# Kernel tuning notes

Measured on AMD Instinct MI355X. Metric: run time of the kernel, lower is better.

## Reference

```python
import jax, jax.numpy as jnp
import numpy as np

IN_F, OUT_F = 4096, 4096
GROUP = 128
N_GROUPS = IN_F // GROUP
R, NUM_A, NUM_B = 16, 2, 2
LORA_ALPHA = 32
SCALING = LORA_ALPHA / R  # 2.0
BITS = 4
PACK = 32 // BITS  # 8 int4 per int32


def dequant_gptq(qweight, qzeros, scales, g_idx):
    """Unpack int4 GPTQ weights -> dense [in_features, out_features] fp32."""
    shifts = (jnp.arange(PACK, dtype=jnp.int32) * BITS)
    # qweight: [in/8, out] packed along in dim
    wq = (qweight[:, None, :] >> shifts[None, :, None]) & 0xF       # [in/8, 8, out]
    wq = wq.reshape(IN_F, OUT_F).astype(jnp.float32)
    # qzeros: [n_groups, out/8] packed along out dim
    zq = (qzeros[:, :, None] >> shifts[None, None, :]) & 0xF        # [g, out/8, 8]
    zq = zq.reshape(N_GROUPS, OUT_F).astype(jnp.float32)
    # per-row group lookup
    return scales[g_idx] * (wq - zq[g_idx])                          # [in, out]


def activation_weights(x, normalize=True):
    # 'inps' mode: per-input-feature importance from mean |activation|
    w = jnp.mean(jnp.abs(x), axis=tuple(range(x.ndim - 1)))          # [in]
    if normalize:
        w = w / (jnp.mean(w) + 1e-6)
    return w


def setup_inputs() -> dict:
    key = jax.random.key(0)
    ks = jax.random.split(key, 8)
    x = jax.random.normal(ks[0], (2, 2048, IN_F), dtype=jnp.float32)
    scales = jax.random.uniform(ks[1], (N_GROUPS, OUT_F), dtype=jnp.float32) * 0.01 + 0.001
    bias = jax.random.normal(ks[2], (OUT_F,), dtype=jnp.float32) * 0.01
    lora_A = jax.random.normal(ks[3], (NUM_A, R, IN_F), dtype=jnp.float32) * (1.0 / np.sqrt(IN_F))
    lora_B = jax.random.normal(ks[4], (NUM_B, OUT_F, R), dtype=jnp.float32) * 0.01
    qweight = jax.random.randint(ks[5], (IN_F // PACK, OUT_F), 0, 2147483647, dtype=jnp.int32)
    qzeros = jax.random.randint(ks[6], (N_GROUPS, OUT_F // PACK), 0, 2147483647, dtype=jnp.int32)
    g_idx = (jnp.arange(IN_F, dtype=jnp.int32) // GROUP).astype(jnp.int32)
    return {"x": x, "scales": scales, "bias": bias, "lora_A": lora_A,
            "lora_B": lora_B, "qweight": qweight, "qzeros": qzeros, "g_idx": g_idx}


def reference(x, scales, bias, lora_A, lora_B, qweight, qzeros, g_idx):
    W = dequant_gptq(qweight, qzeros, scales, g_idx)                 # [in, out]
    result = jnp.einsum('bsi,io->bso', x, W) + bias                  # base GPTQ linear
    # activation-aware 'inps' weighting (dropout p=0 -> identity, eval mode)
    aw = activation_weights(x, normalize=True)                       # [in]
    x_w = x * aw                                                     # broadcast on last dim
    # sum_{i,j} B_j(A_i(x_w)) == (sum_j B_j) @ (sum_i A_i) @ x_w (all linear, no bias)
    A_sum = jnp.sum(lora_A, axis=0)                                  # [r, in]
    B_sum = jnp.sum(lora_B, axis=0)                                  # [out, r]
    h = jnp.einsum('bsi,ri->bsr', x_w, A_sum)                        # [b, s, r]
    result = result + jnp.einsum('bsr,or->bso', h, B_sum) * SCALING
    return result
```

## Files before the change

kernel.cpp:

```cpp
#include <hip/hip_runtime.h>
#include <stdint.h>

#define IN_F 4096
#define OUT_F 4096

typedef __attribute__((ext_vector_type(4))) float f32x4;
typedef _Float16 f16x8 __attribute__((ext_vector_type(8)));
typedef _Float16 f16x2 __attribute__((ext_vector_type(2)));
typedef unsigned short u16x8 __attribute__((ext_vector_type(8)));

__device__ __forceinline__ unsigned short f2h(float f) {
  _Float16 h = (_Float16)f;
  return __builtin_bit_cast(unsigned short, h);
}

#define SIGMA_TAB 0x73625140u

#define OFF_XH     ((size_t)0)
#define OFF_PART   ((size_t)33554432)
#define OFF_W      ((size_t)35651584)
#define OFF_BSUM   ((size_t)35667968)
#define OFF_AW     ((size_t)35668480)
#define OFF_BS     ((size_t)35799552)
#define OFF_HPART  ((size_t)36061696)
#define OFF_HB     ((size_t)38158848)
#define WS_NEED    ((size_t)38420992)

__global__ __launch_bounds__(256) void k1_prep(const float* __restrict__ x,
                                               unsigned short* __restrict__ xh,
                                               float* __restrict__ part) {
  int t = threadIdx.x;
  int c8 = (blockIdx.x * 256 + t) * 8;
  int by = blockIdx.y;
  float a[8];
  #pragma unroll
  for (int i = 0; i < 8; ++i) a[i] = 0.f;
  for (int rr = 0; rr < 32; ++rr) {
    size_t off = (size_t)(by * 32 + rr) * IN_F + c8;
    f32x4 v0 = *(const f32x4*)(x + off);
    f32x4 v1 = *(const f32x4*)(x + off + 4);
    u16x8 o;
    o[0] = f2h(v0[0]); o[1] = f2h(v1[0]); o[2] = f2h(v0[1]); o[3] = f2h(v1[1]);
    o[4] = f2h(v0[2]); o[5] = f2h(v1[2]); o[6] = f2h(v0[3]); o[7] = f2h(v1[3]);
    *(u16x8*)(xh + off) = o;
    a[0] += fabsf(v0[0]); a[1] += fabsf(v0[1]); a[2] += fabsf(v0[2]); a[3] += fabsf(v0[3]);
    a[4] += fabsf(v1[0]); a[5] += fabsf(v1[1]); a[6] += fabsf(v1[2]); a[7] += fabsf(v1[3]);
  }
  f32x4 p0 = { a[0], a[1], a[2], a[3] };
  f32x4 p1 = { a[4], a[5], a[6], a[7] };
  *(f32x4*)(part + (size_t)by * IN_F + c8) = p0;
  *(f32x4*)(part + (size_t)by * IN_F + c8 + 4) = p1;
}

__global__ __launch_bounds__(256) void k2_colred(const float* __restrict__ part,
                                                 float* __restrict__ w,
                                                 float* __restrict__ bsum) {
  int t = threadIdx.x;
  int col = blockIdx.x * 256 + t;
  float s = 0.f;
  for (int st = 0; st < 128; ++st) s += part[(size_t)st * IN_F + col];
  float wv = s * (1.0f / 4096.0f);
  w[col] = wv;
  __shared__ float red[256];
  red[t] = wv; __syncthreads();
  for (int k = 128; k > 0; k >>= 1) { if (t < k) red[t] += red[t + k]; __syncthreads(); }
  if (t == 0) bsum[blockIdx.x] = red[0];
}

__global__ __launch_bounds__(256) void k3_fold(const float* __restrict__ lora_A,
                                               const float* __restrict__ lora_B,
                                               const float* __restrict__ w,
                                               const float* __restrict__ bsum,
                                               unsigned short* __restrict__ A_w,
                                               unsigned short* __restrict__ Bs) {
  int b = blockIdx.x, t = threadIdx.x;
  float s = 0.f;
  #pragma unroll
  for (int i = 0; i < 16; ++i) s += bsum[i];
  float iv = 1.0f / (s * (1.0f / 4096.0f) + 1e-6f);
  if (b < 256) {
    int idx = b * 256 + t;
    int r = idx >> 12;
    int pos = idx & 4095;
    int p = pos & 7;
    int orig = (pos & ~7) + (int)((SIGMA_TAB >> (p * 4)) & 7);
    float v = (lora_A[(size_t)r * IN_F + orig] + lora_A[(size_t)(16 + r) * IN_F + orig]) * w[orig] * iv;
    A_w[idx] = f2h(v);
  } else {
    int idx = (b - 256) * 256 + t;
    int o = idx >> 5, r = idx & 31;
    float v = 0.f;
    if (r < 16) v = 2.0f * (lora_B[o * 16 + r] + lora_B[OUT_F * 16 + o * 16 + r]);
    Bs[idx] = f2h(v);
  }
}

__global__ __launch_bounds__(256) void k4_h(const unsigned short* __restrict__ xh,
                                            const unsigned short* __restrict__ A_w,
                                            float* __restrict__ hpart) {
  int mb = blockIdx.x, kc = blockIdx.y;
  int t = threadIdx.x, wid = t >> 6, l = t & 63;
  int m0 = mb * 128 + wid * 32;
  int lr = l & 15, lg = l >> 4;
  f32x4 z = { 0.f, 0.f, 0.f, 0.f };
  f32x4 acc0 = z, acc1 = z;
  for (int it = 0; it < 16; ++it) {
    int k = kc * 512 + it * 32 + lg * 8;
    f16x8 b  = *(const f16x8*)(A_w + (size_t)lr * IN_F + k);
    f16x8 a0 = *(const f16x8*)(xh + (size_t)(m0 + lr) * IN_F + k);
    f16x8 a1 = *(const f16x8*)(xh + (size_t)(m0 + 16 + lr) * IN_F + k);
    acc0 = __builtin_amdgcn_mfma_f32_16x16x32_f16(a0, b, acc0, 0, 0, 0);
    acc1 = __builtin_amdgcn_mfma_f32_16x16x32_f16(a1, b, acc1, 0, 0, 0);
  }
  float* hp = hpart + (size_t)kc * IN_F * 16;
  #pragma unroll
  for (int r = 0; r < 4; ++r) {
    hp[(size_t)(m0 + lg * 4 + r) * 16 + lr]      = acc0[r];
    hp[(size_t)(m0 + 16 + lg * 4 + r) * 16 + lr] = acc1[r];
  }
}

__global__ __launch_bounds__(256) void k5_hred(const float* __restrict__ hpart,
                                               unsigned short* __restrict__ hb) {
  int gid = blockIdx.x * 256 + threadIdx.x;
  int m = gid >> 5, r = gid & 31;
  float v = 0.f;
  if (r < 16)
    for (int kc = 0; kc < 8; ++kc) v += hpart[(size_t)kc * 65536 + m * 16 + r];
  hb[gid] = f2h(v);
}

__device__ __forceinline__ f16x8 deq8(unsigned int q, f16x2 s2, f16x2 zz2) {
  unsigned int u0 = ( q         & 0x000F000Fu) | 0x64006400u;
  unsigned int u1 = ((q >> 4)   & 0x000F000Fu) | 0x64006400u;
  unsigned int u2 = ((q >> 8)   & 0x000F000Fu) | 0x64006400u;
  unsigned int u3 = ((q >> 12)  & 0x000F000Fu) | 0x64006400u;
  f16x2 w0 = (__builtin_bit_cast(f16x2, u0) - zz2) * s2;
  f16x2 w1 = (__builtin_bit_cast(f16x2, u1) - zz2) * s2;
  f16x2 w2 = (__builtin_bit_cast(f16x2, u2) - zz2) * s2;
  f16x2 w3 = (__builtin_bit_cast(f16x2, u3) - zz2) * s2;
  struct { f16x2 a, b, c, d; } r { w0, w1, w2, w3 };
  return __builtin_bit_cast(f16x8, r);
}

__global__ __launch_bounds__(256) void k6_gemm(const unsigned short* __restrict__ xh,
                                               const int* __restrict__ qweight,
                                               const int* __restrict__ qzeros,
                                               const float* __restrict__ scales,
                                               const float* __restrict__ bias,
                                               const unsigned short* __restrict__ hb,
                                               const unsigned short* __restrict__ Bs,
                                               float* __restrict__ out) {
  __shared__ __align__(16) unsigned short As[2][128 * 64];
  int t = threadIdx.x, w = t >> 6, l = t & 63;
  int lr = l & 15, lg = l >> 4;
  int b0 = blockIdx.x;
  int bid = (b0 & 7) * 128 + (b0 >> 3);
  int mt = bid >> 5, nt = bid & 31;
  int m0 = mt * 128, n0 = nt * 128;
  int ncol0 = n0 + w * 32 + lr;

  f32x4 zz = { 0.f, 0.f, 0.f, 0.f };
  f32x4 acc[8][2];
  #pragma unroll
  for (int m = 0; m < 8; ++m) { acc[m][0] = zz; acc[m][1] = zz; }

  int row0 = t >> 3;
  int cp = (t & 7) ^ (row0 & 7);
  const unsigned short* aE = xh + (size_t)(m0 + row0) * IN_F + cp * 8;
  const int*   qE = qweight + (size_t)lg * OUT_F + ncol0;
  const float* sC = scales + ncol0;
  const int*   zC = qzeros + (ncol0 >> 3);
  int zsh = (lr & 7) * 4;

  #define STAGE_A(BUF, APTR) do {                                                 \
    _Pragma("unroll")                                                             \
    for (int it = 0; it < 4; ++it) {                                              \
      const unsigned short* gp = (APTR) + (size_t)it * 32 * IN_F;                 \
      __builtin_amdgcn_global_load_lds((const __attribute__((address_space(1))) void*)gp, \
                                       (__attribute__((address_space(3))) void*)(&As[BUF][0] + (it * 256 + t) * 8), \
                                       16, 0, 0);                                 \
    }                                                                             \
  } while (0)

  #define LOAD_QW(QW, QPTR) do {                                                  \
    _Pragma("unroll")                                                             \
    for (int ks = 0; ks < 2; ++ks)                                                \
      _Pragma("unroll")                                                           \
      for (int j = 0; j < 2; ++j)                                                 \
        QW[j][ks] = (unsigned int)(QPTR)[ks * 4 * OUT_F + j * 16];                \
  } while (0)

  #define LOAD_CONST(S2, ZP, SPTR, ZPTR) do {                                     \
    _Pragma("unroll")                                                             \
    for (int j = 0; j < 2; ++j) {                                                 \
      float s_ = (SPTR)[j * 16];                                                  \
      unsigned int zi = (unsigned int)(ZPTR)[j * 2];                              \
      unsigned int z = (zi >> zsh) & 0xFu;                                        \
      unsigned int zzu = 0x64006400u + z * 0x00010001u;                           \
      ZP[j] = __builtin_bit_cast(f16x2, zzu);                                     \
      _Float16 sh = (_Float16)s_;                                                 \
      unsigned int sb = (unsigned int)__builtin_bit_cast(unsigned short, sh);     \
      unsigned int ssu = (sb << 16) | sb;                                         \
      S2[j] = __builtin_bit_cast(f16x2, ssu);                                     \
    }                                                                             \
  } while (0)

  #define COMPUTE(BUF, QW, S2, ZP) do {                                           \
    _Pragma("unroll")                                                             \
    for (int ks = 0; ks < 2; ++ks) {                                              \
      f16x8 bf0 = deq8(QW[0][ks], S2[0], ZP[0]);                                  \
      f16x8 bf1 = deq8(QW[1][ks], S2[1], ZP[1]);                                  \
      f16x8 a[8];                                                                 \
      int chunk = (ks * 4 + lg) ^ (lr & 7);                                       \
      _Pragma("unroll")                                                           \
      for (int m = 0; m < 8; ++m)                                                 \
        a[m] = *(const f16x8*)(&As[BUF][0] + (m * 16 + lr) * 64 + chunk * 8);     \
      __builtin_amdgcn_s_setprio(1);                                              \
      _Pragma("unroll")                                                           \
      for (int m = 0; m < 8; ++m) {                                               \
        acc[m][0] = __builtin_amdgcn_mfma_f32_16x16x32_f16(a[m], bf0, acc[m][0], 0, 0, 0); \
        acc[m][1] = __builtin_amdgcn_mfma_f32_16x16x32_f16(a[m], bf1, acc[m][1], 0, 0, 0); \
      }                                                                           \
      __builtin_amdgcn_s_setprio(0);                                              \
    }                                                                             \
  } while (0)

  unsigned int qwA[2][2], qwB[2][2];
  f16x2 s2a[2], zpa[2], s2n[2], zpn[2];

  STAGE_A(0, aE);
  LOAD_QW(qwA, qE);
  LOAD_CONST(s2a, zpa, sC, zC);
  sC += OUT_F; zC += OUT_F / 8;
  const unsigned short* aO = aE + 64;
  const int*   qO = qE + 8 * OUT_F;
  aE += 128; qE += 16 * OUT_F;
  __syncthreads();

  for (int kt = 0; kt < 64; kt += 2) {
    LOAD_QW(qwB, qO);
    STAGE_A(1, aO);
    COMPUTE(0, qwA, s2a, zpa);
    __syncthreads();
    if (kt + 2 < 64) {
      LOAD_QW(qwA, qE);
      LOAD_CONST(s2n, zpn, sC, zC);
      STAGE_A(0, aE);
    }
    COMPUTE(1, qwB, s2a, zpa);
    __syncthreads();
    s2a[0] = s2n[0]; s2a[1] = s2n[1];
    zpa[0] = zpn[0]; zpa[1] = zpn[1];
    sC += OUT_F; zC += OUT_F / 8;
    aO += 128; qO += 16 * OUT_F;
    aE += 128; qE += 16 * OUT_F;
  }
  #undef STAGE_A
  #undef LOAD_QW
  #undef LOAD_CONST
  #undef COMPUTE

  {
    f16x8 bb[2];
    #pragma unroll
    for (int j = 0; j < 2; ++j)
      bb[j] = *(const f16x8*)(Bs + (size_t)(ncol0 + j * 16) * 32 + lg * 8);
    #pragma unroll
    for (int m = 0; m < 8; ++m) {
      f16x8 ah = *(const f16x8*)(hb + (size_t)(m0 + m * 16 + lr) * 32 + lg * 8);
      acc[m][0] = __builtin_amdgcn_mfma_f32_16x16x32_f16(ah, bb[0], acc[m][0], 0, 0, 0);
      acc[m][1] = __builtin_amdgcn_mfma_f32_16x16x32_f16(ah, bb[1], acc[m][1], 0, 0, 0);
    }
  }
  #pragma unroll
  for (int j = 0; j < 2; ++j) {
    int ocol = ncol0 + j * 16;
    float bv = bias[ocol];
    #pragma unroll
    for (int m = 0; m < 8; ++m) {
      int orow = m0 + m * 16 + lg * 4;
      #pragma unroll
      for (int r = 0; r < 4; ++r)
        out[(size_t)(orow + r) * OUT_F + ocol] = acc[m][j][r] + bv;
    }
  }
}

extern "C" void kernel_launch(void* const* d_in, const int* in_sizes, int n_in,
                              void* d_out, int out_size, void* d_ws, size_t ws_size,
                              hipStream_t stream) {
  const float* x       = (const float*)d_in[0];
  const float* scales  = (const float*)d_in[1];
  const float* bias    = (const float*)d_in[2];
  const float* lora_A  = (const float*)d_in[3];
  const float* lora_B  = (const float*)d_in[4];
  const int*   qweight = (const int*)d_in[5];
  const int*   qzeros  = (const int*)d_in[6];
  float* out = (float*)d_out;

  if (ws_size < WS_NEED) return;

  char* ws = (char*)d_ws;
  unsigned short* xh  = (unsigned short*)(ws + OFF_XH);
  float* part         = (float*)(ws + OFF_PART);
  float* w            = (float*)(ws + OFF_W);
  float* bsum         = (float*)(ws + OFF_BSUM);
  unsigned short* A_w = (unsigned short*)(ws + OFF_AW);
  unsigned short* Bs  = (unsigned short*)(ws + OFF_BS);
  float* hpart        = (float*)(ws + OFF_HPART);
  unsigned short* hb  = (unsigned short*)(ws + OFF_HB);

  k1_prep<<<dim3(2, 128), 256, 0, stream>>>(x, xh, part);
  k2_colred<<<16, 256, 0, stream>>>(part, w, bsum);
  k3_fold<<<768, 256, 0, stream>>>(lora_A, lora_B, w, bsum, A_w, Bs);
  k4_h<<<dim3(32, 8), 256, 0, stream>>>(xh, A_w, hpart);
  k5_hred<<<512, 256, 0, stream>>>(hpart, hb);
  k6_gemm<<<1024, 256, 0, stream>>>(xh, qweight, qzeros, scales, bias, hb, Bs, out);
}
```

Baseline: 188.1 us.

## Triple-buffer LDS A tiles with vmcnt-gated barriers in GPTQ GEMM

Replaces the double-buffered LDS staging of activation tiles with a rotating three-buffer scheme. Each half-step now waits on partial vmcnt plus a raw barrier instead of a full __syncthreads, so global loads for the tile two steps ahead can stay in flight during compute. LDS use grows from two to three 16KB buffers, which may lower occupancy. The hand-written vmcnt counts depend on exact load ordering, and scale/zero loads are consumed right after being issued, which may force early waits and undo part of the overlap.

```diff
diff --git a/kernel.cpp b/kernel.cpp
--- a/kernel.cpp
+++ b/kernel.cpp
@@ -151,11 +151,11 @@
                                                const unsigned short* __restrict__ hb,
                                                const unsigned short* __restrict__ Bs,
                                                float* __restrict__ out) {
-  __shared__ __align__(16) unsigned short As[2][128 * 64];
+  __shared__ __align__(16) unsigned short As[3 * 128 * 64];
   int t = threadIdx.x, w = t >> 6, l = t & 63;
   int lr = l & 15, lg = l >> 4;
-  int b0 = blockIdx.x;
-  int bid = (b0 & 7) * 128 + (b0 >> 3);
+  int b0id = blockIdx.x;
+  int bid = (b0id & 7) * 128 + (b0id >> 3);
   int mt = bid >> 5, nt = bid & 31;
   int m0 = mt * 128, n0 = nt * 128;
   int ncol0 = n0 + w * 32 + lr;
@@ -167,18 +167,16 @@
 
   int row0 = t >> 3;
   int cp = (t & 7) ^ (row0 & 7);
-  const unsigned short* aE = xh + (size_t)(m0 + row0) * IN_F + cp * 8;
-  const int*   qE = qweight + (size_t)lg * OUT_F + ncol0;
-  const float* sC = scales + ncol0;
-  const int*   zC = qzeros + (ncol0 >> 3);
+  const unsigned short* aBase = xh + (size_t)(m0 + row0) * IN_F + cp * 8;
+  const int*   qBase = qweight + (size_t)lg * OUT_F + ncol0;
   int zsh = (lr & 7) * 4;
 
-  #define STAGE_A(BUF, APTR) do {                                                 \
+  #define STAGE_A(OFF, APTR) do {                                                 \
     _Pragma("unroll")                                                             \
     for (int it = 0; it < 4; ++it) {                                              \
       const unsigned short* gp = (APTR) + (size_t)it * 32 * IN_F;                 \
       __builtin_amdgcn_global_load_lds((const __attribute__((address_space(1))) void*)gp, \
-                                       (__attribute__((address_space(3))) void*)(&As[BUF][0] + (it * 256 + t) * 8), \
+                                       (__attribute__((address_space(3))) void*)(As + (OFF) + (it * 256 + t) * 8), \
                                        16, 0, 0);                                 \
     }                                                                             \
   } while (0)
@@ -206,7 +204,7 @@
     }                                                                             \
   } while (0)
 
-  #define COMPUTE(BUF, QW, S2, ZP) do {                                           \
+  #define COMPUTE(OFF, QW, S2, ZP) do {                                           \
     _Pragma("unroll")                                                             \
     for (int ks = 0; ks < 2; ++ks) {                                              \
       f16x8 bf0 = deq8(QW[0][ks], S2[0], ZP[0]);                                  \
@@ -215,7 +213,7 @@
       int chunk = (ks * 4 + lg) ^ (lr & 7);                                       \
       _Pragma("unroll")                                                           \
       for (int m = 0; m < 8; ++m)                                                 \
-        a[m] = *(const f16x8*)(&As[BUF][0] + (m * 16 + lr) * 64 + chunk * 8);     \
+        a[m] = *(const f16x8*)(As + (OFF) + (m * 16 + lr) * 64 + chunk * 8);      \
       __builtin_amdgcn_s_setprio(1);                                              \
       _Pragma("unroll")                                                           \
       for (int m = 0; m < 8; ++m) {                                               \
@@ -226,40 +224,58 @@
     }                                                                             \
   } while (0)
 
-  unsigned int qwA[2][2], qwB[2][2];
+  #define WAITBAR(N) do {                                                         \
+    asm volatile("s_waitcnt vmcnt(" #N ")" ::: "memory");                         \
+    __builtin_amdgcn_s_barrier();                                                 \
+    asm volatile("" ::: "memory");                                                \
+  } while (0)
+
+  unsigned int qwE[2][2], qwO[2][2];
   f16x2 s2a[2], zpa[2], s2n[2], zpn[2];
 
-  STAGE_A(0, aE);
-  LOAD_QW(qwA, qE);
-  LOAD_CONST(s2a, zpa, sC, zC);
-  sC += OUT_F; zC += OUT_F / 8;
-  const unsigned short* aO = aE + 64;
-  const int*   qO = qE + 8 * OUT_F;
-  aE += 128; qE += 16 * OUT_F;
-  __syncthreads();
-
-  for (int kt = 0; kt < 64; kt += 2) {
-    LOAD_QW(qwB, qO);
-    STAGE_A(1, aO);
-    COMPUTE(0, qwA, s2a, zpa);
-    __syncthreads();
-    if (kt + 2 < 64) {
-      LOAD_QW(qwA, qE);
-      LOAD_CONST(s2n, zpn, sC, zC);
-      STAGE_A(0, aE);
-    }
-    COMPUTE(1, qwB, s2a, zpa);
-    __syncthreads();
+  STAGE_A(0, aBase);
+  LOAD_QW(qwE, qBase);
+  STAGE_A(8192, aBase + 64);
+  LOAD_QW(qwO, qBase + 8 * OUT_F);
+  LOAD_CONST(s2a, zpa, scales + ncol0, qzeros + (ncol0 >> 3));
+  asm volatile("s_waitcnt vmcnt(0)" ::: "memory");
+  __builtin_amdgcn_s_barrier();
+  asm volatile("" ::: "memory");
+
+  int b0 = 0, b1 = 8192, b2 = 16384;
+  const unsigned short* pSE = aBase + 128;
+  const unsigned short* pSO = aBase + 192;
+  const int*   qSE = qBase + 16 * OUT_F;
+  const int*   qSO = qBase + 24 * OUT_F;
+  const float* sC = scales + ncol0 + OUT_F;
+  const int*   zC = qzeros + (ncol0 >> 3) + OUT_F / 8;
+
+  for (int i = 0; i < 31; ++i) {
+    WAITBAR(8);
+    COMPUTE(b0, qwE, s2a, zpa);
+    STAGE_A(b2, pSE);
+    LOAD_QW(qwE, qSE);
+    WAITBAR(8);
+    COMPUTE(b1, qwO, s2a, zpa);
+    STAGE_A(b0, pSO);
+    LOAD_QW(qwO, qSO);
+    LOAD_CONST(s2n, zpn, sC, zC);
     s2a[0] = s2n[0]; s2a[1] = s2n[1];
     zpa[0] = zpn[0]; zpa[1] = zpn[1];
+    int tmp = b0; b0 = b2; b2 = b1; b1 = tmp;
+    pSE += 128; pSO += 128;
+    qSE += 16 * OUT_F; qSO += 16 * OUT_F;
     sC += OUT_F; zC += OUT_F / 8;
-    aO += 128; qO += 16 * OUT_F;
-    aE += 128; qE += 16 * OUT_F;
-  }
+  }
+  WAITBAR(8);
+  COMPUTE(b0, qwE, s2a, zpa);
+  WAITBAR(0);
+  COMPUTE(b1, qwO, s2a, zpa);
   #undef STAGE_A
   #undef LOAD_QW
   #undef LOAD_CONST
   #undef COMPUTE
+  #undef WAITBAR
 
   {
     f16x8 bb[2];
```

New measurement: 186.0 us. About the same (-1.1%).
